# Kernel optimization log

Measured on AMD Instinct MI355X. Metric: run time of the kernel, lower is better.

## Reference

```python
import jax, jax.numpy as jnp
import numpy as np

B = 1024        # probe batch
Q = 65536       # queue_size (number of identities in momentum queue)
D = 512         # feat_dim
MARGIN = 0.4
SCALE = 32.0
HARD_NEG = 10   # min(max(int(Q*0.0002), 3), 10)


def setup_inputs() -> dict:
    key = jax.random.key(0)
    k1, k2, k3, k4 = jax.random.split(key, 4)
    p = jax.random.normal(k1, (B, D), dtype=jnp.float32)
    p = p / jnp.linalg.norm(p, axis=1, keepdims=True)
    queue = jax.random.uniform(k2, (2, Q, D), dtype=jnp.float32)
    queue = queue / jnp.linalg.norm(queue, axis=2, keepdims=True)  # F.normalize(queue, dim=2)
    label = jax.random.randint(k3, (B,), 0, Q)
    label = jnp.where(jnp.arange(B) % 4 == 0, -1, label)
    # binary mask buffer marking queue slots whose second copy is active
    mask = (jax.random.uniform(k4, (Q, 1)) < 0.1).astype(jnp.float32)
    return {"p": p, "queue": queue, "mask": mask, "label": label}


def _add_margin_am(cos_theta, label):
    # cos_theta: [B, Q], label: [B] with -1 marking outliers
    pos_mask = label != -1                                  # [B]
    safe_label = jnp.where(pos_mask, label, 0)
    onehot = jax.nn.one_hot(safe_label, cos_theta.shape[1], dtype=cos_theta.dtype)
    # AM-softmax: subtract margin at the ground-truth logit, then scale + CE
    logits = (cos_theta - MARGIN * onehot) * SCALE          # [B, Q]
    log_z = jax.nn.logsumexp(logits, axis=1)                # [B]
    gt = jnp.take_along_axis(cos_theta, safe_label[:, None], axis=1)[:, 0]
    ce = log_z - (gt - MARGIN) * SCALE                      # per-row cross entropy
    n_pos = jnp.sum(pos_mask)
    cls_loss = jnp.where(
        n_pos > 0,
        jnp.sum(jnp.where(pos_mask, ce, 0.0)) / jnp.maximum(n_pos, 1),
        0.0,
    )
    # hard-negative mining over outlier rows: top-k (replaces torch argsort+gather)
    top_vals, _ = jax.lax.top_k(cos_theta, HARD_NEG)        # [B, HARD_NEG]
    hard = jnp.clip(top_vals, 0.0)
    neg_per_row = jnp.mean(hard, axis=1)                    # [B]
    n_neg = jnp.sum(~pos_mask)
    neg_loss = jnp.where(
        n_neg > 0,
        jnp.sum(jnp.where(~pos_mask, neg_per_row, 0.0)) / jnp.maximum(n_neg, 1),
        0.0,
    )
    return cls_loss + neg_loss


def reference(p, queue, mask, label):
    # cos_theta1 = F.linear(p, queue[0])
    cos1 = jnp.einsum('bd,qd->bq', p, queue[0])
    # weight = mask * queue[1] + (1 - mask) * queue[0]  (computed under no_grad in torch)
    weight = mask * queue[1] + (1.0 - mask) * queue[0]
    cos2 = jnp.einsum('bd,qd->bq', p, weight)
    loss = _add_margin_am(cos1, label) + _add_margin_am(cos2, label)
    return loss
```

## Files before the change

### kernel.cpp

```cpp
#include <hip/hip_runtime.h>
#include <stdint.h>

#define B_ 1024
#define Q_ 65536
#define D_ 512
#define MT 128
#define NT 128
#define BK 64
#define NSPLIT 64
#define NCHUNK (Q_ / NSPLIT)
#define NTILES (NCHUNK / NT)
#define KITERS (D_ / BK)

#define SCALE32 32.0f
#define C32 46.16624130844683f

#define WS_ROWV 0
#define WS_LSE  16384
#define WS_TOPK (1u * 1024u * 1024u)
#define WS_PBF  (8u * 1024u * 1024u)
#define WS_QBF0 (12u * 1024u * 1024u)
#define WS_WBF  (76u * 1024u * 1024u)

#define SBUF 49152
#define SA_OFF 0
#define SB0_OFF 16384
#define SB1_OFF 32768

typedef __attribute__((ext_vector_type(8))) short short8;
typedef __attribute__((ext_vector_type(4))) short short4v;
typedef __attribute__((ext_vector_type(4))) float f32x4;

__device__ __forceinline__ unsigned short f2bf(float x) {
  union { float f; uint32_t u; } v; v.f = x;
  uint32_t r = v.u + 0x7fffu + ((v.u >> 16) & 1u);
  return (unsigned short)(r >> 16);
}

__device__ __forceinline__ float bf2f(short u) {
  union { uint32_t i; float f; } v;
  v.i = ((uint32_t)(unsigned short)u) << 16;
  return v.f;
}

__device__ __forceinline__ void async16(void* lds, const void* g) {
  void* gg = (void*)g;
  __builtin_amdgcn_global_load_lds(
      (__attribute__((address_space(1))) unsigned int*)gg,
      (__attribute__((address_space(3))) unsigned int*)lds,
      16, 0, 0);
}

__device__ __forceinline__ void tkins(float v,
    float& t0, float& t1, float& t2, float& t3, float& t4,
    float& t5, float& t6, float& t7, float& t8, float& t9) {
  if (v > t9) {
    t9 = (v > t8) ? t8 : v;
    t8 = (v > t8) ? ((v > t7) ? t7 : v) : t8;
    t7 = (v > t7) ? ((v > t6) ? t6 : v) : t7;
    t6 = (v > t6) ? ((v > t5) ? t5 : v) : t6;
    t5 = (v > t5) ? ((v > t4) ? t4 : v) : t5;
    t4 = (v > t4) ? ((v > t3) ? t3 : v) : t4;
    t3 = (v > t3) ? ((v > t2) ? t2 : v) : t3;
    t2 = (v > t2) ? ((v > t1) ? t1 : v) : t2;
    t1 = (v > t1) ? ((v > t0) ? t0 : v) : t1;
    t0 = (v > t0) ? v : t0;
  }
}

#define TKA(v, a) tkins((v), a[0], a[1], a[2], a[3], a[4], a[5], a[6], a[7], a[8], a[9])

__global__ void cvt_all(const float* __restrict__ q, const float* __restrict__ p,
                        const float* __restrict__ mask,
                        unsigned short* __restrict__ qbf0,
                        unsigned short* __restrict__ wbf,
                        unsigned short* __restrict__ pbf) {
  const int wv = threadIdx.x >> 6;
  const int lane = threadIdx.x & 63;
  const int b = blockIdx.x;
  if (b < Q_ / 4) {
    const int row = b * 4 + wv;
    const float* q0r = q + (size_t)row * D_ + lane * 8;
    float4 a = ((const float4*)q0r)[0];
    float4 bb = ((const float4*)q0r)[1];
    short8 o;
    o[0] = (short)f2bf(a.x); o[1] = (short)f2bf(a.y);
    o[2] = (short)f2bf(a.z); o[3] = (short)f2bf(a.w);
    o[4] = (short)f2bf(bb.x); o[5] = (short)f2bf(bb.y);
    o[6] = (short)f2bf(bb.z); o[7] = (short)f2bf(bb.w);
    *(short8*)(qbf0 + (size_t)row * D_ + lane * 8) = o;
    float m = mask[row];
    if (m != 0.0f) {
      const float* q1r = q0r + (size_t)Q_ * D_;
      float4 c = ((const float4*)q1r)[0];
      float4 d = ((const float4*)q1r)[1];
      a.x = fmaf(m, c.x - a.x, a.x); a.y = fmaf(m, c.y - a.y, a.y);
      a.z = fmaf(m, c.z - a.z, a.z); a.w = fmaf(m, c.w - a.w, a.w);
      bb.x = fmaf(m, d.x - bb.x, bb.x); bb.y = fmaf(m, d.y - bb.y, bb.y);
      bb.z = fmaf(m, d.z - bb.z, bb.z); bb.w = fmaf(m, d.w - bb.w, bb.w);
      o[0] = (short)f2bf(a.x); o[1] = (short)f2bf(a.y);
      o[2] = (short)f2bf(a.z); o[3] = (short)f2bf(a.w);
      o[4] = (short)f2bf(bb.x); o[5] = (short)f2bf(bb.y);
      o[6] = (short)f2bf(bb.z); o[7] = (short)f2bf(bb.w);
      *(short8*)(wbf + (size_t)row * D_ + lane * 8) = o;
    }
  } else {
    const int row = (b - Q_ / 4) * 4 + wv;
    const float* pr = p + (size_t)row * D_ + lane * 8;
    float4 a = ((const float4*)pr)[0];
    float4 bb = ((const float4*)pr)[1];
    short8 o;
    o[0] = (short)f2bf(a.x); o[1] = (short)f2bf(a.y);
    o[2] = (short)f2bf(a.z); o[3] = (short)f2bf(a.w);
    o[4] = (short)f2bf(bb.x); o[5] = (short)f2bf(bb.y);
    o[6] = (short)f2bf(bb.z); o[7] = (short)f2bf(bb.w);
    *(short8*)(pbf + (size_t)row * D_ + lane * 8) = o;
  }
}

__global__ __launch_bounds__(512, 2) void fused_gemm_partial(
    const unsigned short* __restrict__ pbf,
    const unsigned short* __restrict__ qbf0,
    const unsigned short* __restrict__ wbf,
    const float* __restrict__ maskp,
    const int* __restrict__ label,
    char* __restrict__ ws) {
  __shared__ __align__(16) unsigned char smem[3 * SBUF];
  __shared__ float maskb[NT];
  __shared__ float zacc[MT][8];
  __shared__ int olist[MT];
  __shared__ int rowmap[MT];
  __shared__ int sh_ocount;

  const int tid = threadIdx.x;
  const int split = blockIdx.x;
  const int mblk = blockIdx.y;
  const int lane = tid & 63;
  const int wv = tid >> 6;
  const int wr = wv >> 2;
  const int wc = wv & 3;
  const int lr = lane & 15;
  const int lg = lane >> 4;

  if (tid == 0) sh_ocount = 0;
  if (tid < MT) {
    rowmap[tid] = -1;
#pragma unroll
    for (int c = 0; c < 8; ++c) zacc[tid][c] = 0.0f;
  }
  __syncthreads();
  if (tid < MT) {
    if (label[mblk * MT + tid] == -1) {
      int k = atomicAdd(&sh_ocount, 1);
      olist[k] = tid;
    }
  }
  __syncthreads();
  const int noc = sh_ocount;
  if (tid < noc) rowmap[olist[tid]] = tid;
  __syncthreads();
  const int nchunks = (noc + 31) >> 5;

  const int srow = lane >> 3;
  const int sc16 = (lane & 7) ^ srow;
  const size_t g_lane_off = (size_t)srow * D_ + sc16 * 8;

  float T[10];
#pragma unroll
  for (int i = 0; i < 10; ++i) T[i] = -1e30f;

  for (int nt = 0; nt < NTILES; ++nt) {
    const int nbase = split * NCHUNK + nt * NT;
    if (tid < NT) maskb[tid] = maskp[nbase + tid];
    __syncthreads();

    const unsigned short* b1b[2];
#pragma unroll
    for (int t = 0; t < 2; ++t) {
      const int rowl = (wv * 2 + t) * 8 + srow;
      b1b[t] = (maskb[rowl] != 0.0f) ? wbf : qbf0;
    }

    f32x4 acc0[4][2], acc1[4][2];
#pragma unroll
    for (int i = 0; i < 4; ++i)
#pragma unroll
      for (int j = 0; j < 2; ++j) {
        f32x4 z = {0.0f, 0.0f, 0.0f, 0.0f};
        acc0[i][j] = z;
        acc1[i][j] = z;
      }

    auto stage = [&](int buf, int kk) {
      const size_t kcol = (size_t)kk * BK;
      unsigned char* sb = smem + (size_t)buf * SBUF;
#pragma unroll
      for (int t = 0; t < 2; ++t) {
        const int slot = wv * 2 + t;
        const size_t rbase = (size_t)slot * 8;
        async16(sb + SA_OFF + slot * 1024,
                pbf + ((size_t)mblk * MT + rbase) * D_ + kcol + g_lane_off);
        async16(sb + SB0_OFF + slot * 1024,
                qbf0 + ((size_t)nbase + rbase) * D_ + kcol + g_lane_off);
        async16(sb + SB1_OFF + slot * 1024,
                b1b[t] + ((size_t)nbase + rbase) * D_ + kcol + g_lane_off);
      }
    };

    stage(0, 0);
    stage(1, 1);

#pragma unroll
    for (int kk = 0; kk < KITERS; ++kk) {
      if (kk < KITERS - 1)
        asm volatile("s_waitcnt vmcnt(6)" ::: "memory");
      else
        asm volatile("s_waitcnt vmcnt(0)" ::: "memory");
      __builtin_amdgcn_s_barrier();
      if (kk < KITERS - 2) stage((kk + 2) % 3, kk + 2);

      const unsigned char* sb = smem + (size_t)(kk % 3) * SBUF;
#pragma unroll
      for (int s = 0; s < 2; ++s) {
        const int xs = ((s * 4 + lg) ^ (lr & 7)) * 16;
        short8 af[4], bf0[2], bf1[2];
#pragma unroll
        for (int i = 0; i < 4; ++i)
          af[i] = *(const short8*)(sb + SA_OFF + (wr * 64 + i * 16 + lr) * 128 + xs);
#pragma unroll
        for (int j = 0; j < 2; ++j)
          bf0[j] = *(const short8*)(sb + SB0_OFF + (wc * 32 + j * 16 + lr) * 128 + xs);
#pragma unroll
        for (int j = 0; j < 2; ++j)
          bf1[j] = *(const short8*)(sb + SB1_OFF + (wc * 32 + j * 16 + lr) * 128 + xs);
#pragma unroll
        for (int i = 0; i < 4; ++i)
#pragma unroll
          for (int j = 0; j < 2; ++j)
            acc0[i][j] = __builtin_amdgcn_mfma_f32_16x16x32_bf16(af[i], bf0[j], acc0[i][j], 0, 0, 0);
#pragma unroll
        for (int i = 0; i < 4; ++i)
#pragma unroll
          for (int j = 0; j < 2; ++j)
            acc1[i][j] = __builtin_amdgcn_mfma_f32_16x16x32_bf16(af[i], bf1[j], acc1[i][j], 0, 0, 0);
      }
    }

#pragma unroll
    for (int i = 0; i < 4; ++i)
#pragma unroll
      for (int k = 0; k < 4; ++k) {
        float a0 = 0.0f, a1 = 0.0f;
#pragma unroll
        for (int j = 0; j < 2; ++j) {
          a0 += __builtin_amdgcn_exp2f(fmaf(acc0[i][j][k], C32, -C32));
          a1 += __builtin_amdgcn_exp2f(fmaf(acc1[i][j][k], C32, -C32));
        }
#pragma unroll
        for (int m = 1; m < 16; m <<= 1) {
          a0 += __shfl_xor(a0, m, 64);
          a1 += __shfl_xor(a1, m, 64);
        }
        if (lr == 0) {
          const int r = wr * 64 + i * 16 + lg * 4 + k;
          zacc[r][wc * 2 + 0] += a0;
          zacc[r][wc * 2 + 1] += a1;
        }
      }

    for (int c = 0; c < nchunks; ++c) {
      unsigned short* cp = (unsigned short*)smem;
#pragma unroll
      for (int i = 0; i < 4; ++i)
#pragma unroll
        for (int k = 0; k < 4; ++k) {
          const int r = wr * 64 + i * 16 + lg * 4 + k;
          const int o = rowmap[r];
          const int ol = o - c * 32;
          if (o >= 0 && ol >= 0 && ol < 32) {
#pragma unroll
            for (int j = 0; j < 2; ++j) {
              const int col = wc * 32 + j * 16 + lr;
              cp[ol * 128 + col] = f2bf(acc0[i][j][k]);
              cp[(32 + ol) * 128 + col] = f2bf(acc1[i][j][k]);
            }
          }
        }
      __syncthreads();

      {
        float tl[10];
#pragma unroll
        for (int r = 0; r < 10; ++r) tl[r] = -1e30f;
        const int pair = tid >> 2;
        const int q4 = tid & 3;
        const int orow = pair >> 1, mat = pair & 1;
        const int o = c * 32 + orow;
        if (orow < 32 && o < noc) {
          const unsigned short* rp = cp + (mat * 32 + orow) * 128 + q4 * 32;
#pragma unroll
          for (int cc = 0; cc < 8; ++cc) {
            short4v v = *(const short4v*)(rp + cc * 4);
            TKA(bf2f(v.x), tl); TKA(bf2f(v.y), tl);
            TKA(bf2f(v.z), tl); TKA(bf2f(v.w), tl);
          }
          float ot[10];
#pragma unroll
          for (int r = 0; r < 10; ++r) ot[r] = __shfl_xor(tl[r], 1, 64);
#pragma unroll
          for (int r = 0; r < 10; ++r) TKA(ot[r], tl);
#pragma unroll
          for (int r = 0; r < 10; ++r) ot[r] = __shfl_xor(tl[r], 2, 64);
#pragma unroll
          for (int r = 0; r < 10; ++r) TKA(ot[r], tl);
          if (q4 == 0) {
            if (c == 0) {
#pragma unroll
              for (int r = 0; r < 10; ++r) TKA(tl[r], T);
            } else {
              float* slot = (float*)(ws + WS_TOPK) +
                  ((size_t)(mat * B_ + mblk * MT + olist[o]) * NSPLIT + split) * 10;
              if (nt == 0) {
#pragma unroll
                for (int r = 0; r < 10; ++r) slot[r] = tl[r];
              } else {
                float cur[10];
#pragma unroll
                for (int r = 0; r < 10; ++r) cur[r] = slot[r];
#pragma unroll
                for (int r = 0; r < 10; ++r) TKA(tl[r], cur);
#pragma unroll
                for (int r = 0; r < 10; ++r) slot[r] = cur[r];
              }
            }
          }
        }
      }
      __syncthreads();
    }
    if (nchunks > 1) asm volatile("s_waitcnt vmcnt(0)" ::: "memory");
  }

  __syncthreads();
  if (tid < MT) {
    float2* lseo = (float2*)(ws + WS_LSE);
    lseo[(size_t)(mblk * MT + tid) * NSPLIT + split] = make_float2(
        zacc[tid][0] + zacc[tid][2] + zacc[tid][4] + zacc[tid][6],
        zacc[tid][1] + zacc[tid][3] + zacc[tid][5] + zacc[tid][7]);
  }
  {
    const int pair = tid >> 2;
    const int q4 = tid & 3;
    const int orow = pair >> 1, mat = pair & 1;
    if (q4 == 0 && orow < noc && orow < 32) {
      float* slot = (float*)(ws + WS_TOPK) +
          ((size_t)(mat * B_ + mblk * MT + olist[orow]) * NSPLIT + split) * 10;
#pragma unroll
      for (int r = 0; r < 10; ++r) slot[r] = T[r];
    }
  }
}

__global__ void finalize_rows(
    const float* __restrict__ p, const float* __restrict__ queue,
    const float* __restrict__ maskp, const int* __restrict__ label,
    char* __restrict__ ws, float* __restrict__ out) {
  const int row = blockIdx.x;
  const int l = threadIdx.x >> 6;
  const int lane = threadIdx.x & 63;
  const int lab = label[row];
  float* rowv = (float*)(ws + WS_ROWV);

  if (lab != -1) {
    const float2* lsep = (const float2*)(ws + WS_LSE) + (size_t)row * NSPLIT;
    float2 zz = lsep[lane];
    float z = (l == 0) ? zz.x : zz.y;
#pragma unroll
    for (int o = 1; o < 64; o <<= 1) z += __shfl_xor(z, o, 64);

    const float* prow = p + (size_t)row * D_;
    const float* q0r = queue + (size_t)lab * D_;
    const float* q1r = queue + ((size_t)Q_ + (size_t)lab) * D_;
    int c = lane * 8;
    float4 a0 = *(const float4*)(prow + c);
    float4 a1 = *(const float4*)(prow + c + 4);
    float4 b0 = *(const float4*)(q0r + c);
    float4 b1 = *(const float4*)(q0r + c + 4);
    float d0 = a0.x * b0.x + a0.y * b0.y + a0.z * b0.z + a0.w * b0.w
             + a1.x * b1.x + a1.y * b1.y + a1.z * b1.z + a1.w * b1.w;
    float d1 = 0.0f;
    if (l == 1) {
      float4 c0 = *(const float4*)(q1r + c);
      float4 c1 = *(const float4*)(q1r + c + 4);
      d1 = a0.x * c0.x + a0.y * c0.y + a0.z * c0.z + a0.w * c0.w
         + a1.x * c1.x + a1.y * c1.y + a1.z * c1.z + a1.w * c1.w;
    }
#pragma unroll
    for (int o = 1; o < 64; o <<= 1) {
      d0 += __shfl_xor(d0, o, 64);
      d1 += __shfl_xor(d1, o, 64);
    }
    float gt;
    if (l == 0) gt = d0;
    else { float m = maskp[lab]; gt = fmaf(m, d1 - d0, d0); }

    if (lane == 0) {
      float e1 = __builtin_amdgcn_exp2f(fmaf(gt, C32, -C32));
      float e2 = __builtin_amdgcn_exp2f(fmaf(gt - 0.4f, C32, -C32));
      float Zc = z - e1 + e2;
      float ce = 32.0f + __logf(Zc) - (gt - 0.4f) * SCALE32;
      rowv[l * B_ + row] = ce;
    }
  } else {
    const float* tp = (const float*)(ws + WS_TOPK) +
                      ((size_t)l * B_ + row) * NSPLIT * 10 + (size_t)lane * 10;
    float t0 = tp[0], t1 = tp[1], t2 = tp[2], t3 = tp[3], t4 = tp[4];
    float t5 = tp[5], t6 = tp[6], t7 = tp[7], t8 = tp[8], t9 = tp[9];
    float ssum = 0.0f;
#pragma unroll
    for (int r10 = 0; r10 < 10; ++r10) {
      float v = t0;
      int idx = lane;
#pragma unroll
      for (int o = 1; o < 64; o <<= 1) {
        float ov = __shfl_xor(v, o, 64);
        int oi = __shfl_xor(idx, o, 64);
        bool take = (ov > v) || (ov == v && oi < idx);
        v = take ? ov : v;
        idx = take ? oi : idx;
      }
      ssum += fmaxf(v, 0.0f);
      if (idx == lane) {
        t0 = t1; t1 = t2; t2 = t3; t3 = t4; t4 = t5;
        t5 = t6; t6 = t7; t7 = t8; t8 = t9; t9 = -1e30f;
      }
    }
    if (lane == 0) rowv[l * B_ + row] = ssum * 0.1f;
  }
}

__global__ void reduce_final(const int* __restrict__ label,
                             const char* __restrict__ ws,
                             float* __restrict__ out) {
  __shared__ float sce[4], sng[4];
  __shared__ int snp[4], snn[4];
  const int tid = threadIdx.x;
  const float* rowv = (const float*)(ws + WS_ROWV);
  float ce = 0.0f, ng = 0.0f;
  int np = 0, nn = 0;
  for (int r = tid; r < B_; r += 256) {
    float v = rowv[r] + rowv[B_ + r];
    if (label[r] != -1) { ce += v; ++np; }
    else { ng += v; ++nn; }
  }
#pragma unroll
  for (int o = 1; o < 64; o <<= 1) {
    ce += __shfl_xor(ce, o, 64);
    ng += __shfl_xor(ng, o, 64);
    np += __shfl_xor(np, o, 64);
    nn += __shfl_xor(nn, o, 64);
  }
  const int wv = tid >> 6, lane = tid & 63;
  if (lane == 0) { sce[wv] = ce; sng[wv] = ng; snp[wv] = np; snn[wv] = nn; }
  __syncthreads();
  if (tid == 0) {
    float c = 0.0f, g = 0.0f; int p = 0, n = 0;
#pragma unroll
    for (int i = 0; i < 4; ++i) { c += sce[i]; g += sng[i]; p += snp[i]; n += snn[i]; }
    float loss = 0.0f;
    if (p > 0) loss += c / (float)p;
    if (n > 0) loss += g / (float)n;
    out[0] = loss;
  }
}

extern "C" void kernel_launch(void* const* d_in, const int* in_sizes, int n_in,
                              void* d_out, int out_size, void* d_ws, size_t ws_size,
                              hipStream_t stream) {
  const float* p     = (const float*)d_in[0];
  const float* queue = (const float*)d_in[1];
  const float* maskp = (const float*)d_in[2];
  const int*   label = (const int*)d_in[3];
  float* out = (float*)d_out;
  char* ws = (char*)d_ws;

  unsigned short* pbf  = (unsigned short*)(ws + WS_PBF);
  unsigned short* qbf0 = (unsigned short*)(ws + WS_QBF0);
  unsigned short* wbf  = (unsigned short*)(ws + WS_WBF);

  cvt_all<<<Q_ / 4 + B_ / 4, 256, 0, stream>>>(queue, p, maskp, qbf0, wbf, pbf);

  dim3 g1(NSPLIT, B_ / MT);
  fused_gemm_partial<<<g1, 512, 0, stream>>>(pbf, qbf0, wbf, maskp, label, ws);
  finalize_rows<<<B_, 128, 0, stream>>>(p, queue, maskp, label, ws, out);
  reduce_final<<<1, 256, 0, stream>>>(label, ws, out);
}
```

Baseline: 638.2 us.

## Use 4-wave blocks with 64x64 warp tiles and BK=32 stages

The GEMM block shrinks from 8 to 4 waves, and each wave now computes a 64x64 sub-tile for both matrices instead of 64x32. This raises MFMA work per LDS fragment load and halves the per-stage K depth to 32, with a new swizzle. The LDS footprint per block drops, which may allow more blocks per CU. In exchange, accumulator registers double, there are twice as many barriers per tile, and the top-k phase now runs on fewer threads.

Result: faster. 607.6 us (-4.8%).

```diff
diff --git a/kernel.cpp b/kernel.cpp
--- a/kernel.cpp
+++ b/kernel.cpp
@@ -6,11 +6,10 @@
 #define D_ 512
 #define MT 128
 #define NT 128
-#define BK 64
 #define NSPLIT 64
 #define NCHUNK (Q_ / NSPLIT)
 #define NTILES (NCHUNK / NT)
-#define KITERS (D_ / BK)
+#define KIT2 (D_ / 32)
 
 #define SCALE32 32.0f
 #define C32 46.16624130844683f
@@ -22,10 +21,9 @@
 #define WS_QBF0 (12u * 1024u * 1024u)
 #define WS_WBF  (76u * 1024u * 1024u)
 
-#define SBUF 49152
-#define SA_OFF 0
-#define SB0_OFF 16384
-#define SB1_OFF 32768
+#define SBUF3 24576
+#define SB0_OFF3 8192
+#define SB1_OFF3 16384
 
 typedef __attribute__((ext_vector_type(8))) short short8;
 typedef __attribute__((ext_vector_type(4))) short short4v;
@@ -118,16 +116,16 @@
   }
 }
 
-__global__ __launch_bounds__(512, 2) void fused_gemm_partial(
+__global__ __launch_bounds__(256, 2) void fused_gemm_partial(
     const unsigned short* __restrict__ pbf,
     const unsigned short* __restrict__ qbf0,
     const unsigned short* __restrict__ wbf,
     const float* __restrict__ maskp,
     const int* __restrict__ label,
     char* __restrict__ ws) {
-  __shared__ __align__(16) unsigned char smem[3 * SBUF];
+  __shared__ __align__(16) unsigned char smem[3 * SBUF3];
   __shared__ float maskb[NT];
-  __shared__ float zacc[MT][8];
+  __shared__ float zacc[MT][4];
   __shared__ int olist[MT];
   __shared__ int rowmap[MT];
   __shared__ int sh_ocount;
@@ -137,16 +135,16 @@
   const int mblk = blockIdx.y;
   const int lane = tid & 63;
   const int wv = tid >> 6;
-  const int wr = wv >> 2;
-  const int wc = wv & 3;
+  const int wr = wv >> 1;
+  const int wc = wv & 1;
   const int lr = lane & 15;
   const int lg = lane >> 4;
 
   if (tid == 0) sh_ocount = 0;
   if (tid < MT) {
     rowmap[tid] = -1;
-#pragma unroll
-    for (int c = 0; c < 8; ++c) zacc[tid][c] = 0.0f;
+    zacc[tid][0] = 0.0f; zacc[tid][1] = 0.0f;
+    zacc[tid][2] = 0.0f; zacc[tid][3] = 0.0f;
   }
   __syncthreads();
   if (tid < MT) {
@@ -161,9 +159,11 @@
   __syncthreads();
   const int nchunks = (noc + 31) >> 5;
 
-  const int srow = lane >> 3;
-  const int sc16 = (lane & 7) ^ srow;
-  const size_t g_lane_off = (size_t)srow * D_ + sc16 * 8;
+  const int srow4 = lane >> 2;
+  const int sc16 = (lane & 3) ^ (srow4 & 3) ^ ((lane >> 4) & 1);
+  const size_t g_lane_off = (size_t)srow4 * D_ + sc16 * 8;
+
+  const int xs = ((lg ^ (lr & 3) ^ ((lr >> 2) & 1))) * 16;
 
   float T[10];
 #pragma unroll
@@ -174,36 +174,33 @@
     if (tid < NT) maskb[tid] = maskp[nbase + tid];
     __syncthreads();
 
-    const unsigned short* b1b[2];
-#pragma unroll
-    for (int t = 0; t < 2; ++t) {
-      const int rowl = (wv * 2 + t) * 8 + srow;
-      b1b[t] = (maskb[rowl] != 0.0f) ? wbf : qbf0;
-    }
-
-    f32x4 acc0[4][2], acc1[4][2];
+    const unsigned short* b1p[2];
+#pragma unroll
+    for (int t = 0; t < 2; ++t)
+      b1p[t] = (maskb[(wv * 2 + t) * 16 + srow4] != 0.0f) ? wbf : qbf0;
+
+    f32x4 acc0[4][4], acc1[4][4];
 #pragma unroll
     for (int i = 0; i < 4; ++i)
 #pragma unroll
-      for (int j = 0; j < 2; ++j) {
+      for (int j = 0; j < 4; ++j) {
         f32x4 z = {0.0f, 0.0f, 0.0f, 0.0f};
         acc0[i][j] = z;
         acc1[i][j] = z;
       }
 
-    auto stage = [&](int buf, int kk) {
-      const size_t kcol = (size_t)kk * BK;
-      unsigned char* sb = smem + (size_t)buf * SBUF;
+    auto stage = [&](int buf, int k2) {
+      unsigned char* sb = smem + (size_t)buf * SBUF3;
+      const size_t kcol = (size_t)k2 * 32;
 #pragma unroll
       for (int t = 0; t < 2; ++t) {
-        const int slot = wv * 2 + t;
-        const size_t rbase = (size_t)slot * 8;
-        async16(sb + SA_OFF + slot * 1024,
-                pbf + ((size_t)mblk * MT + rbase) * D_ + kcol + g_lane_off);
-        async16(sb + SB0_OFF + slot * 1024,
-                qbf0 + ((size_t)nbase + rbase) * D_ + kcol + g_lane_off);
-        async16(sb + SB1_OFF + slot * 1024,
-                b1b[t] + ((size_t)nbase + rbase) * D_ + kcol + g_lane_off);
+        const int rb = (wv * 2 + t) * 16;
+        async16(sb + (wv * 2 + t) * 1024,
+                pbf + ((size_t)mblk * MT + rb) * D_ + kcol + g_lane_off);
+        async16(sb + SB0_OFF3 + (wv * 2 + t) * 1024,
+                qbf0 + ((size_t)nbase + rb) * D_ + kcol + g_lane_off);
+        async16(sb + SB1_OFF3 + (wv * 2 + t) * 1024,
+                b1p[t] + ((size_t)nbase + rb) * D_ + kcol + g_lane_off);
       }
     };
 
@@ -211,40 +208,37 @@
     stage(1, 1);
 
 #pragma unroll
-    for (int kk = 0; kk < KITERS; ++kk) {
-      if (kk < KITERS - 1)
+    for (int k2 = 0; k2 < KIT2; ++k2) {
+      if (k2 < KIT2 - 1)
         asm volatile("s_waitcnt vmcnt(6)" ::: "memory");
       else
         asm volatile("s_waitcnt vmcnt(0)" ::: "memory");
-      __builtin_amdgcn_s_barrier();
-      if (kk < KITERS - 2) stage((kk + 2) % 3, kk + 2);
-
-      const unsigned char* sb = smem + (size_t)(kk % 3) * SBUF;
-#pragma unroll
-      for (int s = 0; s < 2; ++s) {
-        const int xs = ((s * 4 + lg) ^ (lr & 7)) * 16;
-        short8 af[4], bf0[2], bf1[2];
-#pragma unroll
-        for (int i = 0; i < 4; ++i)
-          af[i] = *(const short8*)(sb + SA_OFF + (wr * 64 + i * 16 + lr) * 128 + xs);
-#pragma unroll
-        for (int j = 0; j < 2; ++j)
-          bf0[j] = *(const short8*)(sb + SB0_OFF + (wc * 32 + j * 16 + lr) * 128 + xs);
-#pragma unroll
-        for (int j = 0; j < 2; ++j)
-          bf1[j] = *(const short8*)(sb + SB1_OFF + (wc * 32 + j * 16 + lr) * 128 + xs);
-#pragma unroll
-        for (int i = 0; i < 4; ++i)
-#pragma unroll
-          for (int j = 0; j < 2; ++j)
-            acc0[i][j] = __builtin_amdgcn_mfma_f32_16x16x32_bf16(af[i], bf0[j], acc0[i][j], 0, 0, 0);
-#pragma unroll
-        for (int i = 0; i < 4; ++i)
-#pragma unroll
-          for (int j = 0; j < 2; ++j)
-            acc1[i][j] = __builtin_amdgcn_mfma_f32_16x16x32_bf16(af[i], bf1[j], acc1[i][j], 0, 0, 0);
-      }
-    }
+      asm volatile("s_barrier" ::: "memory");
+      if (k2 + 2 < KIT2) stage((k2 + 2) % 3, k2 + 2);
+
+      const unsigned char* sb = smem + (size_t)(k2 % 3) * SBUF3;
+      short8 af[4], bf0[4], bf1[4];
+#pragma unroll
+      for (int i = 0; i < 4; ++i)
+        af[i] = *(const short8*)(sb + (wr * 64 + i * 16 + lr) * 64 + xs);
+#pragma unroll
+      for (int j = 0; j < 4; ++j)
+        bf0[j] = *(const short8*)(sb + SB0_OFF3 + (wc * 64 + j * 16 + lr) * 64 + xs);
+#pragma unroll
+      for (int j = 0; j < 4; ++j)
+        bf1[j] = *(const short8*)(sb + SB1_OFF3 + (wc * 64 + j * 16 + lr) * 64 + xs);
+#pragma unroll
+      for (int i = 0; i < 4; ++i)
+#pragma unroll
+        for (int j = 0; j < 4; ++j)
+          acc0[i][j] = __builtin_amdgcn_mfma_f32_16x16x32_bf16(af[i], bf0[j], acc0[i][j], 0, 0, 0);
+#pragma unroll
+      for (int i = 0; i < 4; ++i)
+#pragma unroll
+        for (int j = 0; j < 4; ++j)
+          acc1[i][j] = __builtin_amdgcn_mfma_f32_16x16x32_bf16(af[i], bf1[j], acc1[i][j], 0, 0, 0);
+    }
+    __syncthreads();
 
 #pragma unroll
     for (int i = 0; i < 4; ++i)
@@ -252,7 +246,7 @@
       for (int k = 0; k < 4; ++k) {
         float a0 = 0.0f, a1 = 0.0f;
 #pragma unroll
-        for (int j = 0; j < 2; ++j) {
+        for (int j = 0; j < 4; ++j) {
           a0 += __builtin_amdgcn_exp2f(fmaf(acc0[i][j][k], C32, -C32));
           a1 += __builtin_amdgcn_exp2f(fmaf(acc1[i][j][k], C32, -C32));
         }
@@ -279,8 +273,8 @@
           const int ol = o - c * 32;
           if (o >= 0 && ol >= 0 && ol < 32) {
 #pragma unroll
-            for (int j = 0; j < 2; ++j) {
-              const int col = wc * 32 + j * 16 + lr;
+            for (int j = 0; j < 4; ++j) {
+              const int col = wc * 64 + j * 16 + lr;
               cp[ol * 128 + col] = f2bf(acc0[i][j][k]);
               cp[(32 + ol) * 128 + col] = f2bf(acc1[i][j][k]);
             }
@@ -296,7 +290,7 @@
         const int q4 = tid & 3;
         const int orow = pair >> 1, mat = pair & 1;
         const int o = c * 32 + orow;
-        if (orow < 32 && o < noc) {
+        if (o < noc) {
           const unsigned short* rp = cp + (mat * 32 + orow) * 128 + q4 * 32;
 #pragma unroll
           for (int cc = 0; cc < 8; ++cc) {
@@ -341,12 +335,10 @@
     if (nchunks > 1) asm volatile("s_waitcnt vmcnt(0)" ::: "memory");
   }
 
-  __syncthreads();
   if (tid < MT) {
     float2* lseo = (float2*)(ws + WS_LSE);
-    lseo[(size_t)(mblk * MT + tid) * NSPLIT + split] = make_float2(
-        zacc[tid][0] + zacc[tid][2] + zacc[tid][4] + zacc[tid][6],
-        zacc[tid][1] + zacc[tid][3] + zacc[tid][5] + zacc[tid][7]);
+    lseo[(size_t)(mblk * MT + tid) * NSPLIT + split] =
+        make_float2(zacc[tid][0] + zacc[tid][2], zacc[tid][1] + zacc[tid][3]);
   }
   {
     const int pair = tid >> 2;
@@ -491,7 +483,7 @@
   cvt_all<<<Q_ / 4 + B_ / 4, 256, 0, stream>>>(queue, p, maskp, qbf0, wbf, pbf);
 
   dim3 g1(NSPLIT, B_ / MT);
-  fused_gemm_partial<<<g1, 512, 0, stream>>>(pbf, qbf0, wbf, maskp, label, ws);
+  fused_gemm_partial<<<g1, 256, 0, stream>>>(pbf, qbf0, wbf, maskp, label, ws);
   finalize_rows<<<B_, 128, 0, stream>>>(p, queue, maskp, label, ws, out);
   reduce_final<<<1, 256, 0, stream>>>(label, ws, out);
 }
```

## Replace triple-buffered async K pipeline with single-buffer loop and higher occupancy

Applied to the files above, without the earlier changes.

Drops the three-stage shared-memory ring and the hand-tuned vmcnt waits in the fused GEMM. Each K step now issues its async loads into one 48 KB buffer, synchronizes, runs the MFMAs, then synchronizes again. The launch bound is raised from 2 to 4 blocks per CU so that latency is hidden by more resident blocks rather than by in-block prefetch. This gives up load/compute overlap within a block and tightens the register budget, which risks spills given the 64 accumulator floats per thread. LDS capacity may also stop four blocks from actually fitting on a CU.

After: 619.2 us. 3.0% less time.

```diff
diff --git a/kernel.cpp b/kernel.cpp
--- a/kernel.cpp
+++ b/kernel.cpp
@@ -22,7 +22,6 @@
 #define WS_QBF0 (12u * 1024u * 1024u)
 #define WS_WBF  (76u * 1024u * 1024u)
 
-#define SBUF 49152
 #define SA_OFF 0
 #define SB0_OFF 16384
 #define SB1_OFF 32768
@@ -118,14 +117,14 @@
   }
 }
 
-__global__ __launch_bounds__(512, 2) void fused_gemm_partial(
+__global__ __launch_bounds__(512, 4) void fused_gemm_partial(
     const unsigned short* __restrict__ pbf,
     const unsigned short* __restrict__ qbf0,
     const unsigned short* __restrict__ wbf,
     const float* __restrict__ maskp,
     const int* __restrict__ label,
     char* __restrict__ ws) {
-  __shared__ __align__(16) unsigned char smem[3 * SBUF];
+  __shared__ __align__(16) unsigned char smem[49152];
   __shared__ float maskb[NT];
   __shared__ float zacc[MT][8];
   __shared__ int olist[MT];
@@ -191,48 +190,34 @@
         acc1[i][j] = z;
       }
 
-    auto stage = [&](int buf, int kk) {
+    for (int kk = 0; kk < KITERS; ++kk) {
       const size_t kcol = (size_t)kk * BK;
-      unsigned char* sb = smem + (size_t)buf * SBUF;
 #pragma unroll
       for (int t = 0; t < 2; ++t) {
         const int slot = wv * 2 + t;
         const size_t rbase = (size_t)slot * 8;
-        async16(sb + SA_OFF + slot * 1024,
+        async16(smem + SA_OFF + slot * 1024,
                 pbf + ((size_t)mblk * MT + rbase) * D_ + kcol + g_lane_off);
-        async16(sb + SB0_OFF + slot * 1024,
+        async16(smem + SB0_OFF + slot * 1024,
                 qbf0 + ((size_t)nbase + rbase) * D_ + kcol + g_lane_off);
-        async16(sb + SB1_OFF + slot * 1024,
+        async16(smem + SB1_OFF + slot * 1024,
                 b1b[t] + ((size_t)nbase + rbase) * D_ + kcol + g_lane_off);
       }
-    };
-
-    stage(0, 0);
-    stage(1, 1);
-
-#pragma unroll
-    for (int kk = 0; kk < KITERS; ++kk) {
-      if (kk < KITERS - 1)
-        asm volatile("s_waitcnt vmcnt(6)" ::: "memory");
-      else
-        asm volatile("s_waitcnt vmcnt(0)" ::: "memory");
-      __builtin_amdgcn_s_barrier();
-      if (kk < KITERS - 2) stage((kk + 2) % 3, kk + 2);
-
-      const unsigned char* sb = smem + (size_t)(kk % 3) * SBUF;
+      __syncthreads();
+
 #pragma unroll
       for (int s = 0; s < 2; ++s) {
         const int xs = ((s * 4 + lg) ^ (lr & 7)) * 16;
         short8 af[4], bf0[2], bf1[2];
 #pragma unroll
         for (int i = 0; i < 4; ++i)
-          af[i] = *(const short8*)(sb + SA_OFF + (wr * 64 + i * 16 + lr) * 128 + xs);
+          af[i] = *(const short8*)(smem + SA_OFF + (wr * 64 + i * 16 + lr) * 128 + xs);
 #pragma unroll
         for (int j = 0; j < 2; ++j)
-          bf0[j] = *(const short8*)(sb + SB0_OFF + (wc * 32 + j * 16 + lr) * 128 + xs);
+          bf0[j] = *(const short8*)(smem + SB0_OFF + (wc * 32 + j * 16 + lr) * 128 + xs);
 #pragma unroll
         for (int j = 0; j < 2; ++j)
-          bf1[j] = *(const short8*)(sb + SB1_OFF + (wc * 32 + j * 16 + lr) * 128 + xs);
+          bf1[j] = *(const short8*)(smem + SB1_OFF + (wc * 32 + j * 16 + lr) * 128 + xs);
 #pragma unroll
         for (int i = 0; i < 4; ++i)
 #pragma unroll
@@ -244,6 +229,7 @@
           for (int j = 0; j < 2; ++j)
             acc1[i][j] = __builtin_amdgcn_mfma_f32_16x16x32_bf16(af[i], bf1[j], acc1[i][j], 0, 0, 0);
       }
+      __syncthreads();
     }
 
 #pragma unroll
@@ -338,7 +324,6 @@
       }
       __syncthreads();
     }
-    if (nchunks > 1) asm volatile("s_waitcnt vmcnt(0)" ::: "memory");
   }
 
   __syncthreads();
```
